# Kernel optimization log

Measured on AMD Instinct MI355X. Metric: run time of the kernel, lower is better.

The kernel has to match this reference:

```python
import jax, jax.numpy as jnp
import numpy as np

N_QUBITS = 8
N_LAYERS = 4
BATCH = 4096


def _ry(theta):
    # RY(theta) = [[cos(t/2), -sin(t/2)], [sin(t/2), cos(t/2)]]
    c = jnp.cos(theta / 2).astype(jnp.complex64)
    s = jnp.sin(theta / 2).astype(jnp.complex64)
    return jnp.stack([jnp.stack([c, -s], axis=-1),
                      jnp.stack([s, c], axis=-1)], axis=-2)  # (..., 2, 2)


def _rz(theta):
    # RZ(theta) = diag(exp(-i t/2), exp(+i t/2))
    p = jnp.exp(-0.5j * theta.astype(jnp.complex64))
    z = jnp.zeros_like(p)
    return jnp.stack([jnp.stack([p, z], axis=-1),
                      jnp.stack([z, jnp.conj(p)], axis=-1)], axis=-2)


def _apply_1q(state, U, w):
    # state: (B, 2, 2, ..., 2); apply 2x2 unitary U on wire w (axis 1+w).
    st = jnp.moveaxis(state, 1 + w, -1)
    if U.ndim == 3:  # per-sample (batched) gate, U: (B, 2, 2)
        st = jnp.einsum('bij,b...j->b...i', U, st)
    else:            # shared gate, U: (2, 2)
        st = jnp.einsum('ij,b...j->b...i', U, st)
    return jnp.moveaxis(st, -1, 1 + w)


def _apply_cnot(state, c, t):
    # flip target wire t where control wire c is |1>
    st = jnp.moveaxis(state, (1 + c, 1 + t), (-2, -1))
    st = jnp.concatenate([st[..., 0:1, :], st[..., 1:2, ::-1]], axis=-2)
    return jnp.moveaxis(st, (-2, -1), (1 + c, 1 + t))


def _circuit(x, weights):
    B = x.shape[0]
    state = jnp.zeros((B,) + (2,) * N_QUBITS, jnp.complex64)
    state = state.at[(slice(None),) + (0,) * N_QUBITS].set(1.0)  # |0...0>
    # Angle encoding: RY(x_i) on each wire, batched over samples
    for i in range(N_QUBITS):
        state = _apply_1q(state, _ry(x[:, i]), i)
    # Variational layers: CNOT ring then RY/RZ rotations
    for l in range(N_LAYERS):
        for i in range(N_QUBITS):
            state = _apply_cnot(state, i, (i + 1) % N_QUBITS)
        for i in range(N_QUBITS):
            state = _apply_1q(state, _ry(weights[l, i, 0]), i)
            state = _apply_1q(state, _rz(weights[l, i, 1]), i)
    # <Z_0> = P(q0=0) - P(q0=1)
    probs = jnp.sum(jnp.abs(state.reshape(B, 2, -1)) ** 2, axis=-1)
    return (probs[:, 0] - probs[:, 1]).astype(jnp.float32)


def setup_inputs() -> dict:
    key = jax.random.key(0)
    k1, k2 = jax.random.split(key)
    x = jax.random.uniform(k1, (BATCH, N_QUBITS), dtype=jnp.float32) * jnp.pi
    weights = jax.random.normal(k2, (N_LAYERS, N_QUBITS, 2), dtype=jnp.float32) * 0.1
    return {"x": x, "weights": weights}


def reference(x, weights):
    return _circuit(x, weights)
```

## Files before the change

### kernel.cpp

```cpp
#include <hip/hip_runtime.h>

#define NQ 8
#define NL 4
#define BATCH 4096


template <int CTRL>
__device__ __forceinline__ float dppx(float v) {
  return __int_as_float(
      __builtin_amdgcn_update_dpp(0, __float_as_int(v), CTRL, 0xF, 0xF, true));
}

__device__ __forceinline__ float swz16(float v) {
  return __int_as_float(__builtin_amdgcn_ds_swizzle(__float_as_int(v), 0x401F));
}
__device__ __forceinline__ float swz4(float v) {
  return __int_as_float(__builtin_amdgcn_ds_swizzle(__float_as_int(v), 0x101F));
}
__device__ __forceinline__ float bperm(int addr, float v) {
  return __int_as_float(__builtin_amdgcn_ds_bpermute(addr, __float_as_int(v)));
}
__device__ __forceinline__ float rlane(float v, int l) {
  return __int_as_float(__builtin_amdgcn_readlane(__float_as_int(v), l));
}
__device__ __forceinline__ float sxor(float v, unsigned m) {
  return __int_as_float(__float_as_int(v) ^ m);
}

template <int W>
__device__ __forceinline__ float xl(float v, int bp32) {
  if constexpr (W == 0) return bperm(bp32, v);
  else if constexpr (W == 1) return swz16(v);
  else if constexpr (W == 2) return dppx<0x128>(v);
  else if constexpr (W == 3) return swz4(v);
  else if constexpr (W == 4) return dppx<0x4E>(v);
  else return dppx<0xB1>(v);
}

template <int W>
__device__ __forceinline__ void ry_gate(float re[4], float im[4],
                                        float c, float s, unsigned m, int bp32) {
  if constexpr (W <= 5) {
    const float ss = sxor(s, m);
#pragma unroll
    for (int r = 0; r < 4; ++r) {
      float pr = xl<W>(re[r], bp32);
      float pi = xl<W>(im[r], bp32);
      re[r] = c * re[r] + ss * pr;
      im[r] = c * im[r] + ss * pi;
    }
  } else {
    constexpr int mm = 1 << (7 - W);
#pragma unroll
    for (int r = 0; r < 4; ++r) {
      if ((r & mm) == 0) {
        const int r1 = r | mm;
        float a0r = re[r], a1r = re[r1];
        float a0i = im[r], a1i = im[r1];
        re[r]  = c * a0r - s * a1r;
        re[r1] = s * a0r + c * a1r;
        im[r]  = c * a0i - s * a1i;
        im[r1] = s * a0i + c * a1i;
      }
    }
  }
}

template <int W>
__device__ __forceinline__ void rz_gate(float re[4], float im[4],
                                        float c, float s, unsigned m) {
  if constexpr (W <= 5) {
    const float ss = sxor(s, m);
#pragma unroll
    for (int r = 0; r < 4; ++r) {
      float nr = re[r] * c - im[r] * ss;
      float ni = im[r] * c + re[r] * ss;
      re[r] = nr; im[r] = ni;
    }
  } else {
    constexpr int mm = 1 << (7 - W);
#pragma unroll
    for (int r = 0; r < 4; ++r) {
      const float ss = (r & mm) ? s : -s;
      float nr = re[r] * c - im[r] * ss;
      float ni = im[r] * c + re[r] * ss;
      re[r] = nr; im[r] = ni;
    }
  }
}

__device__ __forceinline__ void ring(float re[4], float im[4],
                                     int addr_e, int addr_o, bool p2) {
  const float t0r = p2 ? re[2] : re[0];
  const float t1r = p2 ? re[3] : re[1];
  const float t2r = p2 ? re[1] : re[3];
  const float t3r = p2 ? re[0] : re[2];
  const float t0i = p2 ? im[2] : im[0];
  const float t1i = p2 ? im[3] : im[1];
  const float t2i = p2 ? im[1] : im[3];
  const float t3i = p2 ? im[0] : im[2];
  re[0] = bperm(addr_e, t0r);
  re[1] = bperm(addr_o, t1r);
  re[2] = bperm(addr_e, t2r);
  re[3] = bperm(addr_o, t3r);
  im[0] = bperm(addr_e, t0i);
  im[1] = bperm(addr_o, t1i);
  im[2] = bperm(addr_e, t2i);
  im[3] = bperm(addr_o, t3i);
}

__global__ __launch_bounds__(256, 4) void vqc_kernel(const float* __restrict__ x,
                                                     const float* __restrict__ w,
                                                     float* __restrict__ out) {
  const int lane = (int)(threadIdx.x & 63);
  const int s = (int)((blockIdx.x * blockDim.x + threadIdx.x) >> 6);

  const int gray   = lane ^ (lane >> 1);
  const int addr_e = gray << 2;
  const int addr_o = addr_e ^ 0xC0;
  const bool p2    = (__popc(lane) & 1) != 0;
  const int bp32   = (lane ^ 32) << 2;
  const int bp48   = (lane ^ 48) << 2;

  unsigned sm[8];
#pragma unroll
  for (int W = 0; W < 6; ++W)
    sm[W] = ((lane >> (5 - W)) & 1) ? 0u : 0x80000000u;
  sm[6] = 0u; sm[7] = 0u;

  float sn, cs;
  {
    const float wv = w[lane];
    const float xv = x[(s << 3) | (lane & 7)];
    const float ang = (lane >= 56) ? xv : wv;
    __sincosf(ang * 0.5f, &sn, &cs);
  }

  float re[4], im[4];
  {
    const float f0c = rlane(cs, 56), f0s = rlane(sn, 56);
    const float f1c = rlane(cs, 57), f1s = rlane(sn, 57);
    const float f2c = rlane(cs, 58), f2s = rlane(sn, 58);
    const float f3c = rlane(cs, 59), f3s = rlane(sn, 59);
    const float f4c = rlane(cs, 60), f4s = rlane(sn, 60);
    const float f5c = rlane(cs, 61), f5s = rlane(sn, 61);
    const float f6c = rlane(cs, 62), f6s = rlane(sn, 62);
    const float f7c = rlane(cs, 63), f7s = rlane(sn, 63);
    const int L0  = lane & 1;
    const int L5b = (lane >> 5) & 1;
    const float g2 = (gray & 1) ? f5s : f5c;
    const float g3 = (gray & 2) ? f4s : f4c;
    const float g4 = (gray & 4) ? f3s : f3c;
    const float g5 = (gray & 8) ? f2s : f2c;
    const float Pl = (g2 * g3) * (g4 * g5);
    const int  b6 = ((lane >> 4) & 1) ^ L5b;
    const float h0 = (b6 ? f1s : f1c) * (L5b ? f0s : f0c);
    const float h1 = (b6 ? f1c : f1s) * (L5b ? f0c : f0s);
    const float A0 = Pl * h0, A1 = Pl * h1;
    const float f6a = L0 ? f6s : f6c;
    const float f6b = L0 ? f6c : f6s;
    re[0] = A0 * f7c * f6a;
    re[1] = A1 * f7s * f6a;
    re[2] = A0 * f7s * f6b;
    re[3] = A1 * f7c * f6b;
    im[0] = 0.f; im[1] = 0.f; im[2] = 0.f; im[3] = 0.f;
  }

#define APPLY_ROT(BASE, W) {                                 \
    const float cy = rlane(cs, (BASE) + (W) * 2);            \
    const float sy = rlane(sn, (BASE) + (W) * 2);            \
    const float cz = rlane(cs, (BASE) + (W) * 2 + 1);        \
    const float sz = rlane(sn, (BASE) + (W) * 2 + 1);        \
    ry_gate<W>(re, im, cy, sy, sm[W], bp32);                 \
    rz_gate<W>(re, im, cz, sz, sm[W]); }

  {
    const float cy = rlane(cs, 0), sy = rlane(sn, 0);
    const float cz = rlane(cs, 1), sz = rlane(sn, 1);
    const float ssy = sxor(sy, sm[0]);
#pragma unroll
    for (int r = 0; r < 4; ++r) {
      float p = bperm(bp32, re[r]);
      re[r] = cy * re[r] + ssy * p;
    }
    const float ssz = sxor(sz, sm[0]);
#pragma unroll
    for (int r = 0; r < 4; ++r) {
      im[r] = ssz * re[r];
      re[r] = cz * re[r];
    }
    APPLY_ROT(0, 1) APPLY_ROT(0, 2) APPLY_ROT(0, 3)
    APPLY_ROT(0, 4) APPLY_ROT(0, 5) APPLY_ROT(0, 6) APPLY_ROT(0, 7)
  }

#pragma unroll
  for (int l = 1; l < NL - 1; ++l) {
    ring(re, im, addr_e, addr_o, p2);
    const int base = l * 16;
    APPLY_ROT(base, 0) APPLY_ROT(base, 1) APPLY_ROT(base, 2) APPLY_ROT(base, 3)
    APPLY_ROT(base, 4) APPLY_ROT(base, 5) APPLY_ROT(base, 6) APPLY_ROT(base, 7)
  }
#undef APPLY_ROT

  {
    const float cy = rlane(cs, (NL - 1) * 16);
    const float sy = rlane(sn, (NL - 1) * 16);
    const unsigned pm0 = (unsigned)(__popc(lane & 31) & 1) << 31;
    float acc = 0.f;
#pragma unroll
    for (int r = 0; r < 4; ++r) {
      const unsigned pmr = pm0 ^ (((r == 1) | (r == 2)) ? 0x80000000u : 0u);
      const float ssy = sxor(sy, pmr ^ 0x80000000u);
      const float pr = bperm(bp48, re[r]);
      const float pi = bperm(bp48, im[r]);
      const float nr = cy * re[r] + ssy * pr;
      const float ni = cy * im[r] + ssy * pi;
      const float m2 = nr * nr + ni * ni;
      acc += sxor(m2, pmr);
    }
    acc += dppx<0xB1>(acc);
    acc += dppx<0x4E>(acc);
    acc += swz4(acc);
    acc += dppx<0x128>(acc);
    acc += swz16(acc);
    acc += bperm(bp32, acc);
    if (lane == 0) out[s] = acc;
  }
}

extern "C" void kernel_launch(void* const* d_in, const int* in_sizes, int n_in,
                              void* d_out, int out_size, void* d_ws, size_t ws_size,
                              hipStream_t stream) {
  const float* x = (const float*)d_in[0];
  const float* w = (const float*)d_in[1];
  float* out = (float*)d_out;
  (void)in_sizes; (void)n_in; (void)out_size; (void)d_ws; (void)ws_size;

  dim3 grid(BATCH * 64 / 256), block(256);
  hipLaunchKernelGGL(vqc_kernel, grid, block, 0, stream, x, w, out);
}
```

Baseline: 62.39 us.

## Pack two samples per wavefront with eight amplitudes per lane

Each 64-lane wavefront now simulates two circuit samples, one per 32-lane half, and each lane holds 8 amplitudes instead of 4. Wire 0 moves from a cross-half bpermute to an in-half swizzle, and the final reduction drops one bpermute stage. The grid shrinks by half and launch bounds drop to 2 waves per SIMD to allow the larger register footprint. This is meant to cut the per-sample cost of LDS-based lane exchanges and the per-wave setup overhead, but higher register use lowers occupancy.

```diff
diff --git a/kernel.cpp b/kernel.cpp
--- a/kernel.cpp
+++ b/kernel.cpp
@@ -17,6 +17,9 @@
 __device__ __forceinline__ float swz4(float v) {
   return __int_as_float(__builtin_amdgcn_ds_swizzle(__float_as_int(v), 0x101F));
 }
+__device__ __forceinline__ float swz18(float v) {
+  return __int_as_float(__builtin_amdgcn_ds_swizzle(__float_as_int(v), 0x601F));
+}
 __device__ __forceinline__ float bperm(int addr, float v) {
   return __int_as_float(__builtin_amdgcn_ds_bpermute(addr, __float_as_int(v)));
 }
@@ -28,31 +31,30 @@
 }
 
 template <int W>
-__device__ __forceinline__ float xl(float v, int bp32) {
-  if constexpr (W == 0) return bperm(bp32, v);
-  else if constexpr (W == 1) return swz16(v);
-  else if constexpr (W == 2) return dppx<0x128>(v);
-  else if constexpr (W == 3) return swz4(v);
-  else if constexpr (W == 4) return dppx<0x4E>(v);
+__device__ __forceinline__ float xl(float v) {
+  if constexpr (W == 0) return swz16(v);
+  else if constexpr (W == 1) return dppx<0x128>(v);
+  else if constexpr (W == 2) return swz4(v);
+  else if constexpr (W == 3) return dppx<0x4E>(v);
   else return dppx<0xB1>(v);
 }
 
 template <int W>
-__device__ __forceinline__ void ry_gate(float re[4], float im[4],
-                                        float c, float s, unsigned m, int bp32) {
-  if constexpr (W <= 5) {
+__device__ __forceinline__ void ry_gate(float re[8], float im[8],
+                                        float c, float s, unsigned m) {
+  if constexpr (W <= 4) {
     const float ss = sxor(s, m);
 #pragma unroll
-    for (int r = 0; r < 4; ++r) {
-      float pr = xl<W>(re[r], bp32);
-      float pi = xl<W>(im[r], bp32);
+    for (int r = 0; r < 8; ++r) {
+      float pr = xl<W>(re[r]);
+      float pi = xl<W>(im[r]);
       re[r] = c * re[r] + ss * pr;
       im[r] = c * im[r] + ss * pi;
     }
   } else {
     constexpr int mm = 1 << (7 - W);
 #pragma unroll
-    for (int r = 0; r < 4; ++r) {
+    for (int r = 0; r < 8; ++r) {
       if ((r & mm) == 0) {
         const int r1 = r | mm;
         float a0r = re[r], a1r = re[r1];
@@ -67,12 +69,12 @@
 }
 
 template <int W>
-__device__ __forceinline__ void rz_gate(float re[4], float im[4],
+__device__ __forceinline__ void rz_gate(float re[8], float im[8],
                                         float c, float s, unsigned m) {
-  if constexpr (W <= 5) {
+  if constexpr (W <= 4) {
     const float ss = sxor(s, m);
 #pragma unroll
-    for (int r = 0; r < 4; ++r) {
+    for (int r = 0; r < 8; ++r) {
       float nr = re[r] * c - im[r] * ss;
       float ni = im[r] * c + re[r] * ss;
       re[r] = nr; im[r] = ni;
@@ -80,7 +82,7 @@
   } else {
     constexpr int mm = 1 << (7 - W);
 #pragma unroll
-    for (int r = 0; r < 4; ++r) {
+    for (int r = 0; r < 8; ++r) {
       const float ss = (r & mm) ? s : -s;
       float nr = re[r] * c - im[r] * ss;
       float ni = im[r] * c + re[r] * ss;
@@ -89,81 +91,82 @@
   }
 }
 
-__device__ __forceinline__ void ring(float re[4], float im[4],
-                                     int addr_e, int addr_o, bool p2) {
-  const float t0r = p2 ? re[2] : re[0];
-  const float t1r = p2 ? re[3] : re[1];
-  const float t2r = p2 ? re[1] : re[3];
-  const float t3r = p2 ? re[0] : re[2];
-  const float t0i = p2 ? im[2] : im[0];
-  const float t1i = p2 ? im[3] : im[1];
-  const float t2i = p2 ? im[1] : im[3];
-  const float t3i = p2 ? im[0] : im[2];
-  re[0] = bperm(addr_e, t0r);
-  re[1] = bperm(addr_o, t1r);
-  re[2] = bperm(addr_e, t2r);
-  re[3] = bperm(addr_o, t3r);
-  im[0] = bperm(addr_e, t0i);
-  im[1] = bperm(addr_o, t1i);
-  im[2] = bperm(addr_e, t2i);
-  im[3] = bperm(addr_o, t3i);
-}
-
-__global__ __launch_bounds__(256, 4) void vqc_kernel(const float* __restrict__ x,
+__device__ __forceinline__ void ring2(float re[8], float im[8],
+                                      int addr_e, int addr_o, bool P) {
+  const float t0r = P ? re[4] : re[0], t0i = P ? im[4] : im[0];
+  const float t1r = P ? re[5] : re[1], t1i = P ? im[5] : im[1];
+  const float t2r = P ? re[7] : re[3], t2i = P ? im[7] : im[3];
+  const float t3r = P ? re[6] : re[2], t3i = P ? im[6] : im[2];
+  const float t4r = P ? re[2] : re[6], t4i = P ? im[2] : im[6];
+  const float t5r = P ? re[3] : re[7], t5i = P ? im[3] : im[7];
+  const float t6r = P ? re[1] : re[5], t6i = P ? im[1] : im[5];
+  const float t7r = P ? re[0] : re[4], t7i = P ? im[0] : im[4];
+  re[0] = bperm(addr_e, t0r); re[1] = bperm(addr_o, t1r);
+  re[2] = bperm(addr_e, t2r); re[3] = bperm(addr_o, t3r);
+  re[4] = bperm(addr_e, t4r); re[5] = bperm(addr_o, t5r);
+  re[6] = bperm(addr_e, t6r); re[7] = bperm(addr_o, t7r);
+  im[0] = bperm(addr_e, t0i); im[1] = bperm(addr_o, t1i);
+  im[2] = bperm(addr_e, t2i); im[3] = bperm(addr_o, t3i);
+  im[4] = bperm(addr_e, t4i); im[5] = bperm(addr_o, t5i);
+  im[6] = bperm(addr_e, t6i); im[7] = bperm(addr_o, t7i);
+}
+
+__global__ __launch_bounds__(256, 2) void vqc_kernel(const float* __restrict__ x,
                                                      const float* __restrict__ w,
                                                      float* __restrict__ out) {
   const int lane = (int)(threadIdx.x & 63);
-  const int s = (int)((blockIdx.x * blockDim.x + threadIdx.x) >> 6);
-
-  const int gray   = lane ^ (lane >> 1);
-  const int addr_e = gray << 2;
-  const int addr_o = addr_e ^ 0xC0;
-  const bool p2    = (__popc(lane) & 1) != 0;
-  const int bp32   = (lane ^ 32) << 2;
-  const int bp48   = (lane ^ 48) << 2;
+  const int wv = (int)((blockIdx.x * blockDim.x + threadIdx.x) >> 6);
+  const int hl = lane & 31;
+
+  const int ghl    = hl ^ (hl >> 1);
+  const int addr_e = ((lane & 32) | ghl) << 2;
+  const int addr_o = addr_e ^ 0x60;
+  const bool Ppar  = (__popc(hl) & 1) != 0;
 
   unsigned sm[8];
 #pragma unroll
-  for (int W = 0; W < 6; ++W)
-    sm[W] = ((lane >> (5 - W)) & 1) ? 0u : 0x80000000u;
-  sm[6] = 0u; sm[7] = 0u;
+  for (int W = 0; W < 5; ++W)
+    sm[W] = ((lane >> (4 - W)) & 1) ? 0u : 0x80000000u;
+  sm[5] = 0u; sm[6] = 0u; sm[7] = 0u;
 
   float sn, cs;
   {
-    const float wv = w[lane];
-    const float xv = x[(s << 3) | (lane & 7)];
-    const float ang = (lane >= 56) ? xv : wv;
+    const float wvv = w[lane];
+    const float xv  = x[(wv << 4) | (lane & 15)];
+    const float ang = (lane >= 48) ? xv : wvv;
     __sincosf(ang * 0.5f, &sn, &cs);
   }
-
-  float re[4], im[4];
-  {
-    const float f0c = rlane(cs, 56), f0s = rlane(sn, 56);
-    const float f1c = rlane(cs, 57), f1s = rlane(sn, 57);
-    const float f2c = rlane(cs, 58), f2s = rlane(sn, 58);
-    const float f3c = rlane(cs, 59), f3s = rlane(sn, 59);
-    const float f4c = rlane(cs, 60), f4s = rlane(sn, 60);
-    const float f5c = rlane(cs, 61), f5s = rlane(sn, 61);
-    const float f6c = rlane(cs, 62), f6s = rlane(sn, 62);
-    const float f7c = rlane(cs, 63), f7s = rlane(sn, 63);
-    const int L0  = lane & 1;
-    const int L5b = (lane >> 5) & 1;
-    const float g2 = (gray & 1) ? f5s : f5c;
-    const float g3 = (gray & 2) ? f4s : f4c;
-    const float g4 = (gray & 4) ? f3s : f3c;
-    const float g5 = (gray & 8) ? f2s : f2c;
-    const float Pl = (g2 * g3) * (g4 * g5);
-    const int  b6 = ((lane >> 4) & 1) ^ L5b;
-    const float h0 = (b6 ? f1s : f1c) * (L5b ? f0s : f0c);
-    const float h1 = (b6 ? f1c : f1s) * (L5b ? f0c : f0s);
-    const float A0 = Pl * h0, A1 = Pl * h1;
-    const float f6a = L0 ? f6s : f6c;
-    const float f6b = L0 ? f6c : f6s;
-    re[0] = A0 * f7c * f6a;
-    re[1] = A1 * f7s * f6a;
-    re[2] = A0 * f7s * f6b;
-    re[3] = A1 * f7c * f6b;
-    im[0] = 0.f; im[1] = 0.f; im[2] = 0.f; im[3] = 0.f;
+  float cy48, sy48;
+  __sincosf(w[48] * 0.5f, &sy48, &cy48);
+
+  float fc[8], fs[8];
+  {
+    const int fbase = (48 + ((lane >> 5) << 3)) << 2;
+#pragma unroll
+    for (int k = 0; k < 8; ++k) {
+      fc[k] = bperm(fbase + (k << 2), cs);
+      fs[k] = bperm(fbase + (k << 2), sn);
+    }
+  }
+
+  float re[8], im[8];
+  {
+    const int HL4 = (lane >> 4) & 1, G3 = (ghl >> 3) & 1, HL0 = lane & 1;
+    const float Pl = ((ghl & 4) ? fs[2] : fc[2]) *
+                     ((ghl & 2) ? fs[3] : fc[3]) *
+                     ((ghl & 1) ? fs[4] : fc[4]);
+    const float q0 = (HL4 ? fs[0] : fc[0]) * (G3 ? fs[1] : fc[1]);
+    const float q1 = (HL4 ? fc[0] : fs[0]) * (G3 ? fc[1] : fs[1]);
+    const float g50 = HL0 ? fs[5] : fc[5];
+    const float g51 = HL0 ? fc[5] : fs[5];
+    const float a0 = Pl * q0 * g50, a1 = Pl * q1 * g50;
+    const float b0 = Pl * q0 * g51, b1 = Pl * q1 * g51;
+    const float cc = fc[6] * fc[7], csx = fc[6] * fs[7];
+    const float sc = fs[6] * fc[7], ssx = fs[6] * fs[7];
+    re[0] = a0 * cc;  re[1] = a1 * csx; re[2] = a0 * ssx; re[3] = a1 * sc;
+    re[4] = b0 * sc;  re[5] = b1 * ssx; re[6] = b0 * csx; re[7] = b1 * cc;
+#pragma unroll
+    for (int r = 0; r < 8; ++r) im[r] = 0.f;
   }
 
 #define APPLY_ROT(BASE, W) {                                 \
@@ -171,7 +174,7 @@
     const float sy = rlane(sn, (BASE) + (W) * 2);            \
     const float cz = rlane(cs, (BASE) + (W) * 2 + 1);        \
     const float sz = rlane(sn, (BASE) + (W) * 2 + 1);        \
-    ry_gate<W>(re, im, cy, sy, sm[W], bp32);                 \
+    ry_gate<W>(re, im, cy, sy, sm[W]);                       \
     rz_gate<W>(re, im, cz, sz, sm[W]); }
 
   {
@@ -179,13 +182,13 @@
     const float cz = rlane(cs, 1), sz = rlane(sn, 1);
     const float ssy = sxor(sy, sm[0]);
 #pragma unroll
-    for (int r = 0; r < 4; ++r) {
-      float p = bperm(bp32, re[r]);
+    for (int r = 0; r < 8; ++r) {
+      float p = swz16(re[r]);
       re[r] = cy * re[r] + ssy * p;
     }
     const float ssz = sxor(sz, sm[0]);
 #pragma unroll
-    for (int r = 0; r < 4; ++r) {
+    for (int r = 0; r < 8; ++r) {
       im[r] = ssz * re[r];
       re[r] = cz * re[r];
     }
@@ -195,7 +198,7 @@
 
 #pragma unroll
   for (int l = 1; l < NL - 1; ++l) {
-    ring(re, im, addr_e, addr_o, p2);
+    ring2(re, im, addr_e, addr_o, Ppar);
     const int base = l * 16;
     APPLY_ROT(base, 0) APPLY_ROT(base, 1) APPLY_ROT(base, 2) APPLY_ROT(base, 3)
     APPLY_ROT(base, 4) APPLY_ROT(base, 5) APPLY_ROT(base, 6) APPLY_ROT(base, 7)
@@ -203,28 +206,26 @@
 #undef APPLY_ROT
 
   {
-    const float cy = rlane(cs, (NL - 1) * 16);
-    const float sy = rlane(sn, (NL - 1) * 16);
-    const unsigned pm0 = (unsigned)(__popc(lane & 31) & 1) << 31;
+    const unsigned pm0 = (unsigned)(__popc(lane & 15) & 1) << 31;
     float acc = 0.f;
 #pragma unroll
-    for (int r = 0; r < 4; ++r) {
-      const unsigned pmr = pm0 ^ (((r == 1) | (r == 2)) ? 0x80000000u : 0u);
-      const float ssy = sxor(sy, pmr ^ 0x80000000u);
-      const float pr = bperm(bp48, re[r]);
-      const float pi = bperm(bp48, im[r]);
-      const float nr = cy * re[r] + ssy * pr;
-      const float ni = cy * im[r] + ssy * pi;
-      const float m2 = nr * nr + ni * ni;
-      acc += sxor(m2, pmr);
+    for (int r = 0; r < 8; ++r) {
+      const unsigned podd =
+          ((r == 1) | (r == 2) | (r == 4) | (r == 7)) ? 0x80000000u : 0u;
+      const unsigned pmr = pm0 ^ podd;
+      const float ssy = sxor(sy48, pmr ^ 0x80000000u);
+      const float pr = swz18(re[r]);
+      const float pi = swz18(im[r]);
+      const float nr = cy48 * re[r] + ssy * pr;
+      const float ni = cy48 * im[r] + ssy * pi;
+      acc += sxor(nr * nr + ni * ni, pmr);
     }
     acc += dppx<0xB1>(acc);
     acc += dppx<0x4E>(acc);
     acc += swz4(acc);
     acc += dppx<0x128>(acc);
     acc += swz16(acc);
-    acc += bperm(bp32, acc);
-    if (lane == 0) out[s] = acc;
+    if ((lane & 31) == 0) out[(wv << 1) | (lane >> 5)] = acc;
   }
 }
 
@@ -236,6 +237,6 @@
   float* out = (float*)d_out;
   (void)in_sizes; (void)n_in; (void)out_size; (void)d_ws; (void)ws_size;
 
-  dim3 grid(BATCH * 64 / 256), block(256);
+  dim3 grid(BATCH / 2 * 64 / 256), block(256);
   hipLaunchKernelGGL(vqc_kernel, grid, block, 0, stream, x, w, out);
 }
```

Measured after the change: 61.61 us. About the same (-1.2%).
